# Kernel tuning notes

Hardware: AMD Instinct MI355X
Metric: run time of the kernel (lower is better)

## Reference

```python
import jax, jax.numpy as jnp
import numpy as np


def setup_inputs() -> dict:
    key = jax.random.key(0)
    ks = jax.random.split(key, 6)
    B, H, W, Cin, Cout, wdim = 8, 64, 64, 512, 512, 512
    return {
        "x": jax.random.normal(ks[0], (B, H, W, Cin), jnp.float32),
        "w": jax.random.normal(ks[1], (B, wdim), jnp.float32),
        "noise": jax.random.normal(ks[2], (B, H, W, 1), jnp.float32),
        "style_weight": jax.random.normal(ks[3], (wdim, Cin), jnp.float32),
        "style_bias": jnp.ones((Cin,), jnp.float32),
        "conv_weight": jax.random.normal(ks[4], (3, 3, Cin, Cout), jnp.float32),
        "scale_noise": 0.1 * jax.random.normal(ks[5], (1, 1, 1, Cout), jnp.float32),
        "bias": jax.random.normal(jax.random.fold_in(key, 7), (Cout,), jnp.float32),
    }


def reference(x, w, noise, style_weight, style_bias, conv_weight, scale_noise, bias):
    wdim = style_weight.shape[0]
    kh, kw, cin, cout = conv_weight.shape
    # Equalized-LR fully connected to_style (gain=1, lr_mult=1, bias init ones,
    # activation=True -> leaky_relu(0.2) with sqrt(2) gain, StyleGAN2 convention).
    s = w @ (style_weight * (1.0 / np.sqrt(wdim))) + style_bias  # [B, Cin]
    s = jax.nn.leaky_relu(s, 0.2) * np.sqrt(2.0).astype(np.float32)
    # Modulated conv (demodulated). Equalized-LR weight scale 1/sqrt(fan_in).
    wk = conv_weight * (1.0 / np.sqrt(kh * kw * cin))  # [3,3,Cin,Cout]
    # demod[b,o] = rsqrt(sum_{h,w,i} (wk[h,w,i,o]*s[b,i])^2 + eps)
    d = jax.lax.rsqrt(jnp.einsum('hwio,bi->bo', wk * wk, s * s) + 1e-8)  # [B,Cout]
    xm = x * s[:, None, None, :]  # modulate inputs instead of per-sample weights
    y = jax.lax.conv_general_dilated(
        xm, wk, window_strides=(1, 1), padding='SAME',
        dimension_numbers=('NHWC', 'HWIO', 'NHWC'))
    y = y * d[:, None, None, :]
    # noise scale-add + bias + leaky-relu (the fused tail in StyleGAN2 kernels)
    y = y + scale_noise * noise + bias
    return jax.nn.leaky_relu(y, 0.2)
```

## Files before the change

kernel.cpp:

```cpp
#include <hip/hip_runtime.h>
#include <hip/hip_bf16.h>
#include <stdint.h>


typedef __attribute__((ext_vector_type(8))) __bf16 bf16x8;
typedef __attribute__((ext_vector_type(16))) float f32x16;

__device__ __forceinline__ float bf2f(ushort u) {
    union { uint32_t i; float f; } v; v.i = (uint32_t)u << 16; return v.f;
}
__device__ __forceinline__ ushort f2bf(float f) {
    union { float f; uint32_t i; } v; v.f = f;
    uint32_t r = v.i + 0x7fffu + ((v.i >> 16) & 1u);
    return (ushort)(r >> 16);
}
__device__ __forceinline__ int sniff_f32(const void* sb) {
    return ((const uint32_t*)sb)[0] == 0x3F800000u;
}
__device__ __forceinline__ float lda(const void* p, int idx, int isf) {
    return isf ? ((const float*)p)[idx] : bf2f(((const ushort*)p)[idx]);
}

union U16x8 { uint4 v; ushort u[8]; };

#define INV_SQRT_WDIM 0.04419417382415922f
#define SQRT2         1.4142135623730951f
#define WSCALE        0.014731391274719739f

__global__ void k_style_part(const void* __restrict__ w, const void* __restrict__ sw,
                             const void* __restrict__ sb, float* __restrict__ part) {
    int isf = sniff_f32(sb);
    int b = blockIdx.x >> 3, ds = blockIdx.x & 7;
    int i = threadIdx.x;
    __shared__ float wrow[64];
    if (i < 64) wrow[i] = lda(w, b * 512 + ds * 64 + i, isf);
    __syncthreads();
    float acc = 0.f;
    if (isf) {
        const float* p = (const float*)sw + (size_t)ds * 64 * 512;
#pragma unroll 8
        for (int d = 0; d < 64; ++d) acc += wrow[d] * p[d * 512 + i];
    } else {
        const ushort* p = (const ushort*)sw + (size_t)ds * 64 * 512;
#pragma unroll 8
        for (int d = 0; d < 64; ++d) acc += wrow[d] * bf2f(p[d * 512 + i]);
    }
    part[(b * 8 + ds) * 512 + i] = acc;
}

__global__ void k_style_fin(const float* __restrict__ part, const void* __restrict__ sb,
                            float* __restrict__ s_out) {
    int isf = sniff_f32(sb);
    int b = blockIdx.x, i = threadIdx.x;
    float a = 0.f;
#pragma unroll
    for (int ds = 0; ds < 8; ++ds) a += part[(b * 8 + ds) * 512 + i];
    float s = a * INV_SQRT_WDIM + lda(sb, i, isf);
    s = (s > 0.f ? s : 0.2f * s) * SQRT2;
    s_out[b * 512 + i] = s;
}

__global__ void k_pad(const void* __restrict__ x, const float* __restrict__ s,
                      const void* __restrict__ sb, ushort* __restrict__ xmp) {
    int isf = sniff_f32(sb);
    int pr = blockIdx.x;
    int b = pr / 66, yp = pr % 66;
    int tid = threadIdx.x;
    ushort* rowp = xmp + ((size_t)b * 66 + yp) * 66 * 512;
    uint4 z = {0u, 0u, 0u, 0u};
    if (yp == 0 || yp == 65) {
        uint4* p = (uint4*)rowp;
        for (int l = tid; l < 66 * 512 * 2 / 16; l += 256) p[l] = z;
        return;
    }
    __shared__ float sv[512];
    for (int c = tid; c < 512; c += 256) sv[c] = s[b * 512 + c];
    if (tid < 64)       ((uint4*)rowp)[tid] = z;
    else if (tid < 128) ((uint4*)(rowp + 65 * 512))[tid - 64] = z;
    __syncthreads();
    int y = yp - 1;
    ushort* xout = rowp + 512;
    if (isf) {
        const float* xin = (const float*)x + ((size_t)b * 64 + y) * 64 * 512;
        for (int l = tid; l < 8192; l += 256) {
            int xi = l >> 7, cc = (l & 127) * 4;
            float4 in = *(const float4*)(xin + (size_t)xi * 512 + cc);
            ushort4 ov;
            ov.x = f2bf(in.x * sv[cc + 0]);
            ov.y = f2bf(in.y * sv[cc + 1]);
            ov.z = f2bf(in.z * sv[cc + 2]);
            ov.w = f2bf(in.w * sv[cc + 3]);
            *(ushort4*)(xout + (size_t)xi * 512 + cc) = ov;
        }
    } else {
        const ushort* xin = (const ushort*)x + ((size_t)b * 64 + y) * 64 * 512;
        for (int l = tid; l < 4096; l += 256) {
            int xi = l >> 6, cc = (l & 63) * 8;
            U16x8 in, ov;
            in.v = *(const uint4*)(xin + (size_t)xi * 512 + cc);
#pragma unroll
            for (int j = 0; j < 8; ++j) ov.u[j] = f2bf(bf2f(in.u[j]) * sv[cc + j]);
            *(uint4*)(xout + (size_t)xi * 512 + cc) = ov.v;
        }
    }
}

__global__ void k_wt(const void* __restrict__ cw, const void* __restrict__ sb,
                     ushort* __restrict__ wkt2) {
    int isf = sniff_f32(sb);
    int bid = blockIdx.x;
    int t = bid / 64, ckg = bid % 64;
    __shared__ ushort sm[8][512];
    int tid = threadIdx.x;
#pragma unroll
    for (int r = 0; r < 16; ++r) {
        int l = r * 256 + tid;
        int j = l >> 9, o = l & 511;
        float v = lda(cw, (size_t)(t * 512 + ckg * 8 + j) * 512 + o, isf);
        sm[j][o] = f2bf(v * WSCALE);
    }
    __syncthreads();
#pragma unroll
    for (int r = 0; r < 2; ++r) {
        int o = r * 256 + tid;
        U16x8 pk;
#pragma unroll
        for (int j = 0; j < 8; ++j) pk.u[j] = sm[j][o];
        *(uint4*)(wkt2 + ((size_t)(t * 64 + ckg) * 512 + o) * 8) = pk.v;
    }
}

__global__ void k_dmod(const void* __restrict__ cw, const void* __restrict__ sb,
                       const float* __restrict__ s, float* __restrict__ part) {
    int isf = sniff_f32(sb);
    int t = blockIdx.x / 8, ob = blockIdx.x % 8;
    int tid = threadIdx.x;
    __shared__ float s2[4096];
    __shared__ float red[2048];
#pragma unroll
    for (int j = 0; j < 16; ++j) {
        int idx = j * 256 + tid;
        float v = s[idx];
        s2[idx] = v * v;
    }
    __syncthreads();
    int q = tid >> 6, ol = tid & 63;
    int o = ob * 64 + ol;
    float acc[8] = {0, 0, 0, 0, 0, 0, 0, 0};
    for (int ii = 0; ii < 128; ++ii) {
        int i = q * 128 + ii;
        float wf = lda(cw, (size_t)(t * 512 + i) * 512 + o, isf) * WSCALE;
        float w2 = wf * wf;
#pragma unroll
        for (int b = 0; b < 8; ++b) acc[b] += w2 * s2[b * 512 + i];
    }
#pragma unroll
    for (int b = 0; b < 8; ++b) red[(ol * 8 + b) * 4 + q] = acc[b];
    __syncthreads();
#pragma unroll
    for (int p = 0; p < 2; ++p) {
        int qq = tid * 2 + p;
        int ol2 = qq >> 3, b2 = qq & 7;
        float sum = red[qq * 4 + 0] + red[qq * 4 + 1] + red[qq * 4 + 2] + red[qq * 4 + 3];
        part[(b2 * 9 + t) * 512 + ob * 64 + ol2] = sum;
    }
}

__global__ void k_dfin(const float* __restrict__ part, float* __restrict__ d) {
    int gid = blockIdx.x * 256 + threadIdx.x;
    int b = gid >> 9, o = gid & 511;
    float acc = 1e-8f;
#pragma unroll
    for (int t = 0; t < 9; ++t) acc += part[(b * 9 + t) * 512 + o];
    d[b * 512 + o] = rsqrtf(acc);
}

#define GLL(gp, lp) __builtin_amdgcn_global_load_lds( \
    (const __attribute__((address_space(1))) void*)(gp), \
    (__attribute__((address_space(3))) void*)(lp), 16, 0, 0)
#define VW(n) asm volatile("s_waitcnt vmcnt(" #n ")" ::: "memory")

__launch_bounds__(256, 2)
__global__ void k_conv(const ushort* __restrict__ xmp, const ushort* __restrict__ wkt2,
                       const float* __restrict__ dmod, const void* __restrict__ noise,
                       const void* __restrict__ snoise, const void* __restrict__ bias_,
                       const void* __restrict__ sb, void* __restrict__ out) {
    __shared__ ushort Ah[2][1584 * 8];
    __shared__ ushort Bb[3][512 * 8];
    int isf = sniff_f32(sb);
    int id = blockIdx.x;
    int ct = id & 3;
    int rt = (id >> 2) & 15;
    int b  = id >> 6;
    int y0 = rt * 4, o0 = ct * 128;
    int tid = threadIdx.x;
    int lane = tid & 63, wv = tid >> 6;
    int wr = wv >> 1, wc = wv & 1;
    int lm = lane & 31, kh = lane >> 5;
    const ushort* xb = xmp + (size_t)b * 66 * 66 * 512;
    const ushort* wp = wkt2;

    uint aoff[7];
#pragma unroll
    for (int it = 0; it < 7; ++it) {
        int chunk = (it < 6) ? (it * 256 + tid) : (1536 + wv * 12 + lane);
        int ck = chunk / 396;
        int rem = chunk - ck * 396;
        int hr = rem / 66, cl = rem - hr * 66;
        aoff[it] = (uint)(((y0 + hr) * 66 + cl) * 512 + ck * 8);
    }
    uint boff[2];
#pragma unroll
    for (int it = 0; it < 2; ++it) {
        int L = it * 256 + tid;
        boff[it] = (uint)(((L >> 7) * 512 + o0 + (L & 127)) * 8);
    }

    auto stageA = [&](int c0a, int abuf) {
        char* dstA = (char*)Ah[abuf];
#pragma unroll
        for (int it = 0; it < 6; ++it)
            GLL(xb + aoff[it] + c0a, dstA + (it * 256 + tid) * 16);
        if (lane < 12)
            GLL(xb + aoff[6] + c0a, dstA + (1536 + wv * 12 + lane) * 16);
    };
    auto stageB = [&](int pb, int slot) {
        char* dstB = (char*)Bb[slot];
#pragma unroll
        for (int it = 0; it < 2; ++it)
            GLL(wp + (size_t)pb * 4096 + boff[it], dstB + (it * 256 + tid) * 16);
    };

    f32x16 acc[4][2] = {};

    stageA(0, 0);
    stageB(0 * 64 + 0, 0);
    stageB(1 * 64 + 0, 1);
    VW(2);
    __builtin_amdgcn_s_barrier();
    __builtin_amdgcn_sched_barrier(0);

    for (int c = 0; c < 16; ++c) {
        int c0 = c * 32;
#pragma unroll
        for (int t = 0; t < 9; ++t) {
            if (!(c == 15 && t >= 7)) {
                int tt2 = (t <= 6) ? (t + 2) : (t - 7);
                int cc2 = (t <= 6) ? c : (c + 1);
                stageB(tt2 * 64 + cc2 * 4, (t + 2) % 3);
            }
            if (t == 0 && c < 15) stageA(c0 + 32, (c + 1) & 1);

            const char* AhC = (const char*)Ah[c & 1];
            const char* BbC = (const char*)Bb[t % 3];
            int dy = t / 3 - 1, dx = t % 3 - 1;
            __builtin_amdgcn_s_setprio(1);
#pragma unroll
            for (int ks = 0; ks < 2; ++ks) {
                bf16x8 afr[4], bfr[2];
#pragma unroll
                for (int am = 0; am < 4; ++am)
                    afr[am] = *(const bf16x8*)(AhC + (ks * 2 + kh) * 6336
                        + (wr * 2 + (am >> 1) + dy + 1) * 1056
                        + ((am & 1) * 32 + lm + dx + 1) * 16);
#pragma unroll
                for (int bn = 0; bn < 2; ++bn)
                    bfr[bn] = *(const bf16x8*)(BbC + (ks * 2 + kh) * 2048
                        + (wc * 64 + bn * 32 + lm) * 16);
#pragma unroll
                for (int am = 0; am < 4; ++am)
#pragma unroll
                    for (int bn = 0; bn < 2; ++bn)
                        acc[am][bn] = __builtin_amdgcn_mfma_f32_32x32x16_bf16(
                            afr[am], bfr[bn], acc[am][bn], 0, 0, 0);
            }
            __builtin_amdgcn_s_setprio(0);

            if (t <= 1)      { if (c < 15) { VW(9); } else { VW(2); } }
            else if (t <= 6) { VW(2); }
            else if (t == 7) { if (c < 15) { VW(2); } else { VW(0); } }
            else             { if (c < 15) { VW(2); } }
            if (!(c == 15 && t == 8)) {
                __builtin_amdgcn_s_barrier();
                __builtin_amdgcn_sched_barrier(0);
            }
        }
    }

    float dv[2], snv[2], bv[2];
#pragma unroll
    for (int bn = 0; bn < 2; ++bn) {
        int o = o0 + wc * 64 + bn * 32 + lm;
        dv[bn] = dmod[b * 512 + o];
        snv[bn] = lda(snoise, o, isf);
        bv[bn] = lda(bias_, o, isf);
    }
#pragma unroll
    for (int am = 0; am < 4; ++am) {
#pragma unroll
        for (int reg = 0; reg < 16; ++reg) {
            int crow = 4 * kh + (reg & 3) + 8 * (reg >> 2);
            int yy = y0 + wr * 2 + (am >> 1);
            int xx = (am & 1) * 32 + crow;
            float nz = lda(noise, (b * 64 + yy) * 64 + xx, isf);
            size_t obase = ((size_t)(b * 64 + yy) * 64 + xx) * 512;
            if (isf) {
                float* of = (float*)out;
#pragma unroll
                for (int bn = 0; bn < 2; ++bn) {
                    float v = acc[am][bn][reg] * dv[bn] + snv[bn] * nz + bv[bn];
                    v = v > 0.f ? v : 0.2f * v;
                    of[obase + o0 + wc * 64 + bn * 32 + lm] = v;
                }
            } else {
                ushort* ob = (ushort*)out;
#pragma unroll
                for (int bn = 0; bn < 2; ++bn) {
                    float v = acc[am][bn][reg] * dv[bn] + snv[bn] * nz + bv[bn];
                    v = v > 0.f ? v : 0.2f * v;
                    ob[obase + o0 + wc * 64 + bn * 32 + lm] = f2bf(v);
                }
            }
        }
    }
}

extern "C" void kernel_launch(void* const* d_in, const int* in_sizes, int n_in,
                              void* d_out, int out_size, void* d_ws, size_t ws_size,
                              hipStream_t stream) {
    const void* x     = d_in[0];
    const void* w     = d_in[1];
    const void* noise = d_in[2];
    const void* sw    = d_in[3];
    const void* sb    = d_in[4];
    const void* cw    = d_in[5];
    const void* sn    = d_in[6];
    const void* bias  = d_in[7];

    char* ws = (char*)d_ws;
    ushort* xmp   = (ushort*)(ws);
    ushort* wkt2  = (ushort*)(ws + 35684352);
    float*  s     = (float*)(ws + 40402944);
    float*  dmod  = (float*)(ws + 40419328);
    float*  part  = (float*)(ws + 40435712);
    float*  spart = (float*)(ws + 40583168);
    (void)in_sizes; (void)n_in; (void)out_size; (void)ws_size;

    hipLaunchKernelGGL(k_style_part, dim3(64),     dim3(512), 0, stream, w, sw, sb, spart);
    hipLaunchKernelGGL(k_style_fin,  dim3(8),      dim3(512), 0, stream, spart, sb, s);
    hipLaunchKernelGGL(k_wt,         dim3(576),    dim3(256), 0, stream, cw, sb, wkt2);
    hipLaunchKernelGGL(k_dmod,       dim3(72),     dim3(256), 0, stream, cw, sb, s, part);
    hipLaunchKernelGGL(k_dfin,       dim3(16),     dim3(256), 0, stream, part, dmod);
    hipLaunchKernelGGL(k_pad,        dim3(8 * 66), dim3(256), 0, stream, x, s, sb, xmp);
    hipLaunchKernelGGL(k_conv,       dim3(512),    dim3(256), 0, stream,
                       xmp, wkt2, dmod, noise, sn, bias, sb, d_out);
}
```

Baseline: 337.7 us.

## Fuse prep kernels and restage conv with register-held weights, channel-major input

Merges style finalize, weight transpose, demod and pad into one multi-role prep kernel, and folds the demod rsqrt into the conv epilogue, cutting launches from seven to three. The padded input is stored channel-group-major (16 channels per group), so each conv K-step stages a small A tile in LDS. B fragments now load straight from global memory into registers, triple-buffered across taps, replacing the LDS B ring and its hand-tuned vmcnt waits. This trades LDS traffic for global-latency exposure and more barriers (32 K-steps instead of 16 A stages), and the style vector is recomputed redundantly in many prep blocks.

```diff
diff --git a/kernel.cpp b/kernel.cpp
--- a/kernel.cpp
+++ b/kernel.cpp
@@ -48,145 +48,152 @@
     part[(b * 8 + ds) * 512 + i] = acc;
 }
 
-__global__ void k_style_fin(const float* __restrict__ part, const void* __restrict__ sb,
-                            float* __restrict__ s_out) {
-    int isf = sniff_f32(sb);
-    int b = blockIdx.x, i = threadIdx.x;
+__device__ __forceinline__ float style_s(const float* __restrict__ spart,
+                                         const void* __restrict__ sb,
+                                         int b, int i, int isf) {
     float a = 0.f;
 #pragma unroll
-    for (int ds = 0; ds < 8; ++ds) a += part[(b * 8 + ds) * 512 + i];
+    for (int ds = 0; ds < 8; ++ds) a += spart[(b * 8 + ds) * 512 + i];
     float s = a * INV_SQRT_WDIM + lda(sb, i, isf);
-    s = (s > 0.f ? s : 0.2f * s) * SQRT2;
-    s_out[b * 512 + i] = s;
-}
-
-__global__ void k_pad(const void* __restrict__ x, const float* __restrict__ s,
-                      const void* __restrict__ sb, ushort* __restrict__ xmp) {
-    int isf = sniff_f32(sb);
-    int pr = blockIdx.x;
-    int b = pr / 66, yp = pr % 66;
-    int tid = threadIdx.x;
-    ushort* rowp = xmp + ((size_t)b * 66 + yp) * 66 * 512;
-    uint4 z = {0u, 0u, 0u, 0u};
-    if (yp == 0 || yp == 65) {
-        uint4* p = (uint4*)rowp;
-        for (int l = tid; l < 66 * 512 * 2 / 16; l += 256) p[l] = z;
-        return;
-    }
-    __shared__ float sv[512];
-    for (int c = tid; c < 512; c += 256) sv[c] = s[b * 512 + c];
-    if (tid < 64)       ((uint4*)rowp)[tid] = z;
-    else if (tid < 128) ((uint4*)(rowp + 65 * 512))[tid - 64] = z;
-    __syncthreads();
-    int y = yp - 1;
-    ushort* xout = rowp + 512;
-    if (isf) {
-        const float* xin = (const float*)x + ((size_t)b * 64 + y) * 64 * 512;
-        for (int l = tid; l < 8192; l += 256) {
-            int xi = l >> 7, cc = (l & 127) * 4;
-            float4 in = *(const float4*)(xin + (size_t)xi * 512 + cc);
-            ushort4 ov;
-            ov.x = f2bf(in.x * sv[cc + 0]);
-            ov.y = f2bf(in.y * sv[cc + 1]);
-            ov.z = f2bf(in.z * sv[cc + 2]);
-            ov.w = f2bf(in.w * sv[cc + 3]);
-            *(ushort4*)(xout + (size_t)xi * 512 + cc) = ov;
-        }
-    } else {
-        const ushort* xin = (const ushort*)x + ((size_t)b * 64 + y) * 64 * 512;
-        for (int l = tid; l < 4096; l += 256) {
-            int xi = l >> 6, cc = (l & 63) * 8;
-            U16x8 in, ov;
-            in.v = *(const uint4*)(xin + (size_t)xi * 512 + cc);
-#pragma unroll
-            for (int j = 0; j < 8; ++j) ov.u[j] = f2bf(bf2f(in.u[j]) * sv[cc + j]);
-            *(uint4*)(xout + (size_t)xi * 512 + cc) = ov.v;
-        }
-    }
-}
-
-__global__ void k_wt(const void* __restrict__ cw, const void* __restrict__ sb,
-                     ushort* __restrict__ wkt2) {
+    return (s > 0.f ? s : 0.2f * s) * SQRT2;
+}
+
+__global__ void k_prep(const void* __restrict__ cw, const void* __restrict__ x,
+                       const float* __restrict__ spart, const void* __restrict__ sb,
+                       ushort* __restrict__ wkt2, ushort* __restrict__ xmp2,
+                       float* __restrict__ part) {
     int isf = sniff_f32(sb);
     int bid = blockIdx.x;
-    int t = bid / 64, ckg = bid % 64;
-    __shared__ ushort sm[8][512];
     int tid = threadIdx.x;
-#pragma unroll
-    for (int r = 0; r < 16; ++r) {
-        int l = r * 256 + tid;
-        int j = l >> 9, o = l & 511;
-        float v = lda(cw, (size_t)(t * 512 + ckg * 8 + j) * 512 + o, isf);
-        sm[j][o] = f2bf(v * WSCALE);
-    }
-    __syncthreads();
-#pragma unroll
-    for (int r = 0; r < 2; ++r) {
-        int o = r * 256 + tid;
-        U16x8 pk;
-#pragma unroll
-        for (int j = 0; j < 8; ++j) pk.u[j] = sm[j][o];
-        *(uint4*)(wkt2 + ((size_t)(t * 64 + ckg) * 512 + o) * 8) = pk.v;
-    }
-}
-
-__global__ void k_dmod(const void* __restrict__ cw, const void* __restrict__ sb,
-                       const float* __restrict__ s, float* __restrict__ part) {
-    int isf = sniff_f32(sb);
-    int t = blockIdx.x / 8, ob = blockIdx.x % 8;
-    int tid = threadIdx.x;
+    __shared__ ushort smw[8][512];
+    __shared__ float sv[512];
     __shared__ float s2[4096];
     __shared__ float red[2048];
-#pragma unroll
-    for (int j = 0; j < 16; ++j) {
-        int idx = j * 256 + tid;
-        float v = s[idx];
-        s2[idx] = v * v;
-    }
-    __syncthreads();
-    int q = tid >> 6, ol = tid & 63;
-    int o = ob * 64 + ol;
-    float acc[8] = {0, 0, 0, 0, 0, 0, 0, 0};
-    for (int ii = 0; ii < 128; ++ii) {
-        int i = q * 128 + ii;
-        float wf = lda(cw, (size_t)(t * 512 + i) * 512 + o, isf) * WSCALE;
-        float w2 = wf * wf;
-#pragma unroll
-        for (int b = 0; b < 8; ++b) acc[b] += w2 * s2[b * 512 + i];
-    }
-#pragma unroll
-    for (int b = 0; b < 8; ++b) red[(ol * 8 + b) * 4 + q] = acc[b];
-    __syncthreads();
-#pragma unroll
-    for (int p = 0; p < 2; ++p) {
-        int qq = tid * 2 + p;
-        int ol2 = qq >> 3, b2 = qq & 7;
-        float sum = red[qq * 4 + 0] + red[qq * 4 + 1] + red[qq * 4 + 2] + red[qq * 4 + 3];
-        part[(b2 * 9 + t) * 512 + ob * 64 + ol2] = sum;
-    }
-}
-
-__global__ void k_dfin(const float* __restrict__ part, float* __restrict__ d) {
-    int gid = blockIdx.x * 256 + threadIdx.x;
-    int b = gid >> 9, o = gid & 511;
-    float acc = 1e-8f;
-#pragma unroll
-    for (int t = 0; t < 9; ++t) acc += part[(b * 9 + t) * 512 + o];
-    d[b * 512 + o] = rsqrtf(acc);
+
+    if (bid < 576) {
+        int t = bid / 64, ckg = bid % 64;
+#pragma unroll
+        for (int r = 0; r < 16; ++r) {
+            int l = r * 256 + tid;
+            int j = l >> 9, o = l & 511;
+            float v = lda(cw, (size_t)(t * 512 + ckg * 8 + j) * 512 + o, isf);
+            smw[j][o] = f2bf(v * WSCALE);
+        }
+        __syncthreads();
+#pragma unroll
+        for (int r = 0; r < 2; ++r) {
+            int o = r * 256 + tid;
+            U16x8 pk;
+#pragma unroll
+            for (int j = 0; j < 8; ++j) pk.u[j] = smw[j][o];
+            *(uint4*)(wkt2 + ((size_t)(t * 64 + ckg) * 512 + o) * 8) = pk.v;
+        }
+        return;
+    }
+    if (bid < 1104) {
+        int pr = bid - 576;
+        int b = pr / 66, yp = pr % 66;
+        ushort* xb2 = xmp2 + (size_t)b * 2230272;
+        uint4 z = {0u, 0u, 0u, 0u};
+        if (yp == 0 || yp == 65) {
+            for (int l = tid; l < 4224; l += 256) {
+                int h = l / 132, cc = l - h * 132;
+                *(uint4*)(xb2 + (size_t)(h * 66 + yp) * 1056 + cc * 8) = z;
+            }
+            return;
+        }
+        for (int i = tid; i < 512; i += 256) sv[i] = style_s(spart, sb, b, i, isf);
+        __syncthreads();
+        int y = yp - 1;
+#pragma unroll
+        for (int r = 0; r < 8; ++r) {
+            int u = r * 256 + tid;
+            int col = (u & 63) + 1, h = u >> 6;
+            ushort* op = xb2 + ((size_t)(h * 66 + yp) * 66 + col) * 16;
+            U16x8 o0_, o1_;
+            if (isf) {
+                const float* xin = (const float*)x
+                    + (((size_t)(b * 64 + y)) * 64 + (col - 1)) * 512 + h * 16;
+                float4 f0 = *(const float4*)(xin + 0);
+                float4 f1 = *(const float4*)(xin + 4);
+                float4 f2 = *(const float4*)(xin + 8);
+                float4 f3 = *(const float4*)(xin + 12);
+                const float* sp = sv + h * 16;
+                o0_.u[0] = f2bf(f0.x * sp[0]);  o0_.u[1] = f2bf(f0.y * sp[1]);
+                o0_.u[2] = f2bf(f0.z * sp[2]);  o0_.u[3] = f2bf(f0.w * sp[3]);
+                o0_.u[4] = f2bf(f1.x * sp[4]);  o0_.u[5] = f2bf(f1.y * sp[5]);
+                o0_.u[6] = f2bf(f1.z * sp[6]);  o0_.u[7] = f2bf(f1.w * sp[7]);
+                o1_.u[0] = f2bf(f2.x * sp[8]);  o1_.u[1] = f2bf(f2.y * sp[9]);
+                o1_.u[2] = f2bf(f2.z * sp[10]); o1_.u[3] = f2bf(f2.w * sp[11]);
+                o1_.u[4] = f2bf(f3.x * sp[12]); o1_.u[5] = f2bf(f3.y * sp[13]);
+                o1_.u[6] = f2bf(f3.z * sp[14]); o1_.u[7] = f2bf(f3.w * sp[15]);
+            } else {
+                const ushort* xin = (const ushort*)x
+                    + (((size_t)(b * 64 + y)) * 64 + (col - 1)) * 512 + h * 16;
+                U16x8 i0, i1;
+                i0.v = *(const uint4*)(xin);
+                i1.v = *(const uint4*)(xin + 8);
+                const float* sp = sv + h * 16;
+#pragma unroll
+                for (int j = 0; j < 8; ++j) o0_.u[j] = f2bf(bf2f(i0.u[j]) * sp[j]);
+#pragma unroll
+                for (int j = 0; j < 8; ++j) o1_.u[j] = f2bf(bf2f(i1.u[j]) * sp[8 + j]);
+            }
+            *(uint4*)(op) = o0_.v;
+            *(uint4*)(op + 8) = o1_.v;
+        }
+        if (tid < 64) {
+            int h = tid & 31, side = tid >> 5;
+            ushort* op = xb2 + ((size_t)(h * 66 + yp) * 66 + side * 65) * 16;
+            *(uint4*)(op) = z;
+            *(uint4*)(op + 8) = z;
+        }
+        return;
+    }
+    {
+        int q2 = bid - 1104;
+        int t = q2 / 8, ob = q2 % 8;
+#pragma unroll
+        for (int j = 0; j < 16; ++j) {
+            int idx = j * 256 + tid;
+            int bb = idx >> 9, i = idx & 511;
+            float scv = style_s(spart, sb, bb, i, isf);
+            s2[idx] = scv * scv;
+        }
+        __syncthreads();
+        int q = tid >> 6, ol = tid & 63;
+        int o = ob * 64 + ol;
+        float accd[8] = {0, 0, 0, 0, 0, 0, 0, 0};
+        for (int ii = 0; ii < 128; ++ii) {
+            int i = q * 128 + ii;
+            float wf = lda(cw, (size_t)(t * 512 + i) * 512 + o, isf) * WSCALE;
+            float w2 = wf * wf;
+#pragma unroll
+            for (int bb = 0; bb < 8; ++bb) accd[bb] += w2 * s2[bb * 512 + i];
+        }
+#pragma unroll
+        for (int bb = 0; bb < 8; ++bb) red[(ol * 8 + bb) * 4 + q] = accd[bb];
+        __syncthreads();
+#pragma unroll
+        for (int p = 0; p < 2; ++p) {
+            int u = tid * 2 + p;
+            int ol2 = u >> 3, b2 = u & 7;
+            float sum = red[u * 4 + 0] + red[u * 4 + 1] + red[u * 4 + 2] + red[u * 4 + 3];
+            part[(b2 * 9 + t) * 512 + ob * 64 + ol2] = sum;
+        }
+    }
 }
 
 #define GLL(gp, lp) __builtin_amdgcn_global_load_lds( \
     (const __attribute__((address_space(1))) void*)(gp), \
     (__attribute__((address_space(3))) void*)(lp), 16, 0, 0)
-#define VW(n) asm volatile("s_waitcnt vmcnt(" #n ")" ::: "memory")
 
 __launch_bounds__(256, 2)
-__global__ void k_conv(const ushort* __restrict__ xmp, const ushort* __restrict__ wkt2,
-                       const float* __restrict__ dmod, const void* __restrict__ noise,
+__global__ void k_conv(const ushort* __restrict__ xmp2, const ushort* __restrict__ wkt2,
+                       const float* __restrict__ part, const void* __restrict__ noise,
                        const void* __restrict__ snoise, const void* __restrict__ bias_,
                        const void* __restrict__ sb, void* __restrict__ out) {
-    __shared__ ushort Ah[2][1584 * 8];
-    __shared__ ushort Bb[3][512 * 8];
+    __shared__ ushort Ah[2][6336];
     int isf = sniff_f32(sb);
     int id = blockIdx.x;
     int ct = id & 3;
@@ -197,101 +204,77 @@
     int lane = tid & 63, wv = tid >> 6;
     int wr = wv >> 1, wc = wv & 1;
     int lm = lane & 31, kh = lane >> 5;
-    const ushort* xb = xmp + (size_t)b * 66 * 66 * 512;
-    const ushort* wp = wkt2;
-
-    uint aoff[7];
-#pragma unroll
-    for (int it = 0; it < 7; ++it) {
-        int chunk = (it < 6) ? (it * 256 + tid) : (1536 + wv * 12 + lane);
-        int ck = chunk / 396;
-        int rem = chunk - ck * 396;
-        int hr = rem / 66, cl = rem - hr * 66;
-        aoff[it] = (uint)(((y0 + hr) * 66 + cl) * 512 + ck * 8);
-    }
-    uint boff[2];
-#pragma unroll
-    for (int it = 0; it < 2; ++it) {
-        int L = it * 256 + tid;
-        boff[it] = (uint)(((L >> 7) * 512 + o0 + (L & 127)) * 8);
-    }
-
-    auto stageA = [&](int c0a, int abuf) {
-        char* dstA = (char*)Ah[abuf];
-#pragma unroll
-        for (int it = 0; it < 6; ++it)
-            GLL(xb + aoff[it] + c0a, dstA + (it * 256 + tid) * 16);
-        if (lane < 12)
-            GLL(xb + aoff[6] + c0a, dstA + (1536 + wv * 12 + lane) * 16);
+    const ushort* xb2 = xmp2 + (size_t)b * 2230272;
+    const ushort* wB = wkt2 + kh * 4096 + (size_t)(o0 + wc * 64 + lm) * 8;
+
+    auto stageA = [&](int hp, int buf) {
+        char* dst = (char*)Ah[buf];
+#pragma unroll
+        for (int it = 0; it < 3; ++it) {
+            int L = it * 256 + tid;
+            int hr = L / 132, rem = L - hr * 132;
+            GLL(xb2 + (size_t)(hp * 66 + y0 + hr) * 1056 + rem * 8, dst + L * 16);
+        }
+        if (tid < 24) {
+            int L = 768 + tid;
+            int rem = L - 660;
+            GLL(xb2 + (size_t)(hp * 66 + y0 + 5) * 1056 + rem * 8, dst + L * 16);
+        }
     };
-    auto stageB = [&](int pb, int slot) {
-        char* dstB = (char*)Bb[slot];
-#pragma unroll
-        for (int it = 0; it < 2; ++it)
-            GLL(wp + (size_t)pb * 4096 + boff[it], dstB + (it * 256 + tid) * 16);
+    auto loadB = [&](int t, int h, bf16x8 (&d)[2]) {
+        const ushort* p = wB + (size_t)t * 262144 + h * 8192;
+        d[0] = *(const bf16x8*)(p);
+        d[1] = *(const bf16x8*)(p + 256);
     };
 
     f32x16 acc[4][2] = {};
+    bf16x8 b0[2], b1[2], b2[2];
 
     stageA(0, 0);
-    stageB(0 * 64 + 0, 0);
-    stageB(1 * 64 + 0, 1);
-    VW(2);
-    __builtin_amdgcn_s_barrier();
-    __builtin_amdgcn_sched_barrier(0);
-
-    for (int c = 0; c < 16; ++c) {
-        int c0 = c * 32;
-#pragma unroll
-        for (int t = 0; t < 9; ++t) {
-            if (!(c == 15 && t >= 7)) {
-                int tt2 = (t <= 6) ? (t + 2) : (t - 7);
-                int cc2 = (t <= 6) ? c : (c + 1);
-                stageB(tt2 * 64 + cc2 * 4, (t + 2) % 3);
-            }
-            if (t == 0 && c < 15) stageA(c0 + 32, (c + 1) & 1);
-
-            const char* AhC = (const char*)Ah[c & 1];
-            const char* BbC = (const char*)Bb[t % 3];
+    loadB(0, 0, b0);
+    loadB(1, 0, b1);
+    loadB(2, 0, b2);
+    __syncthreads();
+
+#pragma unroll 1
+    for (int h = 0; h < 32; ++h) {
+        const char* AhC = (const char*)Ah[h & 1];
+        auto tap = [&](int t, const bf16x8 (&bf)[2]) {
             int dy = t / 3 - 1, dx = t % 3 - 1;
-            __builtin_amdgcn_s_setprio(1);
-#pragma unroll
-            for (int ks = 0; ks < 2; ++ks) {
-                bf16x8 afr[4], bfr[2];
-#pragma unroll
-                for (int am = 0; am < 4; ++am)
-                    afr[am] = *(const bf16x8*)(AhC + (ks * 2 + kh) * 6336
-                        + (wr * 2 + (am >> 1) + dy + 1) * 1056
-                        + ((am & 1) * 32 + lm + dx + 1) * 16);
+            bf16x8 afr[4];
+#pragma unroll
+            for (int am = 0; am < 4; ++am)
+                afr[am] = *(const bf16x8*)(AhC
+                    + (wr * 2 + (am >> 1) + dy + 1) * 2112
+                    + ((am & 1) * 32 + lm + dx + 1) * 32 + kh * 16);
+#pragma unroll
+            for (int am = 0; am < 4; ++am)
 #pragma unroll
                 for (int bn = 0; bn < 2; ++bn)
-                    bfr[bn] = *(const bf16x8*)(BbC + (ks * 2 + kh) * 2048
-                        + (wc * 64 + bn * 32 + lm) * 16);
-#pragma unroll
-                for (int am = 0; am < 4; ++am)
-#pragma unroll
-                    for (int bn = 0; bn < 2; ++bn)
-                        acc[am][bn] = __builtin_amdgcn_mfma_f32_32x32x16_bf16(
-                            afr[am], bfr[bn], acc[am][bn], 0, 0, 0);
-            }
-            __builtin_amdgcn_s_setprio(0);
-
-            if (t <= 1)      { if (c < 15) { VW(9); } else { VW(2); } }
-            else if (t <= 6) { VW(2); }
-            else if (t == 7) { if (c < 15) { VW(2); } else { VW(0); } }
-            else             { if (c < 15) { VW(2); } }
-            if (!(c == 15 && t == 8)) {
-                __builtin_amdgcn_s_barrier();
-                __builtin_amdgcn_sched_barrier(0);
-            }
-        }
+                    acc[am][bn] = __builtin_amdgcn_mfma_f32_32x32x16_bf16(
+                        afr[am], bf[bn], acc[am][bn], 0, 0, 0);
+        };
+        tap(0, b0); loadB(3, h, b0);
+        if (h < 31) stageA(h + 1, (h + 1) & 1);
+        tap(1, b1); loadB(4, h, b1);
+        tap(2, b2); loadB(5, h, b2);
+        tap(3, b0); loadB(6, h, b0);
+        tap(4, b1); loadB(7, h, b1);
+        tap(5, b2); loadB(8, h, b2);
+        tap(6, b0); if (h < 31) loadB(0, h + 1, b0);
+        tap(7, b1); if (h < 31) loadB(1, h + 1, b1);
+        tap(8, b2); if (h < 31) loadB(2, h + 1, b2);
+        if (h < 31) __syncthreads();
     }
 
     float dv[2], snv[2], bv[2];
 #pragma unroll
     for (int bn = 0; bn < 2; ++bn) {
         int o = o0 + wc * 64 + bn * 32 + lm;
-        dv[bn] = dmod[b * 512 + o];
+        float a = 1e-8f;
+#pragma unroll
+        for (int t = 0; t < 9; ++t) a += part[(b * 9 + t) * 512 + o];
+        dv[bn] = rsqrtf(a);
         snv[bn] = lda(snoise, o, isf);
         bv[bn] = lda(bias_, o, isf);
     }
@@ -338,20 +321,15 @@
     const void* bias  = d_in[7];
 
     char* ws = (char*)d_ws;
-    ushort* xmp   = (ushort*)(ws);
+    ushort* xmp2  = (ushort*)(ws);
     ushort* wkt2  = (ushort*)(ws + 35684352);
-    float*  s     = (float*)(ws + 40402944);
-    float*  dmod  = (float*)(ws + 40419328);
     float*  part  = (float*)(ws + 40435712);
     float*  spart = (float*)(ws + 40583168);
     (void)in_sizes; (void)n_in; (void)out_size; (void)ws_size;
 
-    hipLaunchKernelGGL(k_style_part, dim3(64),     dim3(512), 0, stream, w, sw, sb, spart);
-    hipLaunchKernelGGL(k_style_fin,  dim3(8),      dim3(512), 0, stream, spart, sb, s);
-    hipLaunchKernelGGL(k_wt,         dim3(576),    dim3(256), 0, stream, cw, sb, wkt2);
-    hipLaunchKernelGGL(k_dmod,       dim3(72),     dim3(256), 0, stream, cw, sb, s, part);
-    hipLaunchKernelGGL(k_dfin,       dim3(16),     dim3(256), 0, stream, part, dmod);
-    hipLaunchKernelGGL(k_pad,        dim3(8 * 66), dim3(256), 0, stream, x, s, sb, xmp);
-    hipLaunchKernelGGL(k_conv,       dim3(512),    dim3(256), 0, stream,
-                       xmp, wkt2, dmod, noise, sn, bias, sb, d_out);
-}
+    hipLaunchKernelGGL(k_style_part, dim3(64),   dim3(512), 0, stream, w, sw, sb, spart);
+    hipLaunchKernelGGL(k_prep,       dim3(1176), dim3(256), 0, stream,
+                       cw, x, spart, sb, wkt2, xmp2, part);
+    hipLaunchKernelGGL(k_conv,       dim3(512),  dim3(256), 0, stream,
+                       xmp2, wkt2, part, noise, sn, bias, sb, d_out);
+}
```

Result: faster. 306.8 us (-9.1%).
